# Kernel optimization log

Hardware: AMD Instinct MI355X
Metric: run time of the kernel (lower is better)

## Reference

```python
import jax, jax.numpy as jnp
import numpy as np

N = 8192
BOX = 50.0
CUTOFF = 5.0
MAX_E = 64 * N  # padded edge capacity (~34 avg neighbors expected)


def setup_inputs() -> dict:
    key = jax.random.key(0)
    pos = jax.random.uniform(key, (N, 3), dtype=jnp.float32) * BOX
    return {"pos": pos}


def _pairwise_dist(pos):
    # Euclidean cdist via the gram-matrix identity; avoids the [N,N,3] intermediate.
    sq = jnp.sum(pos * pos, axis=-1)                      # [N]
    d2 = sq[:, None] + sq[None, :] - 2.0 * (pos @ pos.T)  # [N,N]
    return jnp.sqrt(jnp.maximum(d2, 0.0))


def reference(pos):
    n = pos.shape[0]
    dist = _pairwise_dist(pos)
    # mask self-edges by pushing the diagonal above the cutoff (as in the torch code)
    dist = dist + (CUTOFF + 1.0) * jnp.eye(n, dtype=dist.dtype)
    mask = dist < CUTOFF
    # data-dependent nonzero -> fixed-size padded output for jit compatibility;
    # padded entries are filled with -1.
    rows, cols = jnp.nonzero(mask, size=MAX_E, fill_value=-1)
    return jnp.stack([rows, cols], axis=0)  # [2, MAX_E], int32
```

## Files before the change

### kernel.cpp

```cpp
#include <hip/hip_runtime.h>
#include <stdint.h>

#define N 8192
#define MAX_E (64 * N)
#define NCHUNK (N / 64)
#define NCOL1 9
#define NCELLS (NCOL1 * NCOL1 * NCOL1)
#define CAP 40
#define SCALE (9.0f / 50.0f)
#define POISON 0xAAAAAAAAu
#define M_WAVES 4
#define E_BLOCKS 256
#define E_ROWS 32

__device__ __forceinline__ float sq_exact(float x, float y, float z) {
    return __fadd_rn(__fadd_rn(__fmul_rn(x, x), __fmul_rn(y, y)), __fmul_rn(z, z));
}

__device__ __forceinline__ bool edge_pred(float xi, float yi, float zi, float sqi,
                                          const float4& pj) {
    float dot = __fmaf_rn(zi, pj.z, __fmaf_rn(yi, pj.y, __fmul_rn(xi, pj.x)));
    float d2  = __fmaf_rn(-2.0f, dot, __fadd_rn(sqi, pj.w));
    return d2 < 0x1.8ffffep+4f;
}

__device__ __forceinline__ int cell_of(float v) {
    int c = (int)(__fmul_rn(v, SCALE));
    return c > 8 ? 8 : c;
}

__device__ __forceinline__ int cell3_of(float x, float y, float z) {
    return (cell_of(x) * NCOL1 + cell_of(y)) * NCOL1 + cell_of(z);
}

__global__ __launch_bounds__(256) void bin_kernel(const float* __restrict__ posf,
                                                  unsigned* __restrict__ gcount,
                                                  float4* __restrict__ colpts,
                                                  int* __restrict__ colidx) {
    const int i = blockIdx.x * 256 + threadIdx.x;
    float x = posf[3 * i], y = posf[3 * i + 1], z = posf[3 * i + 2];
    const int cell = cell3_of(x, y, z);
    unsigned p = atomicAdd(&gcount[cell], 1u) - POISON;
    if (p < CAP) {
        colpts[cell * CAP + p] = make_float4(x, y, z, sq_exact(x, y, z));
        colidx[cell * CAP + p] = i;
    }
}

__global__ __launch_bounds__(256) void mask_kernel(const float* __restrict__ posf,
                                                   const unsigned* __restrict__ gcount,
                                                   const float4* __restrict__ colpts,
                                                   const int* __restrict__ colidx,
                                                   uint64_t* __restrict__ masks,
                                                   int* __restrict__ counts,
                                                   int* __restrict__ out) {
    __shared__ uint32_t lmask[M_WAVES][256];
    const int tid  = threadIdx.x;
    const int wave = tid >> 6;
    const int lane = tid & 63;
    const int row  = blockIdx.x * M_WAVES + wave;

    int2 neg; neg.x = -1; neg.y = -1;
    ((int2*)out)[blockIdx.x * 256 + tid] = neg;

#pragma unroll
    for (int k = lane; k < 256; k += 64) lmask[wave][k] = 0;
    __builtin_amdgcn_wave_barrier();

    const float xi = posf[3 * row], yi = posf[3 * row + 1], zi = posf[3 * row + 2];
    const float sqi = sq_exact(xi, yi, zi);
    const int cx = cell_of(xi), cy = cell_of(yi), cz = cell_of(zi);
    const int zlo = (cz > 0) ? cz - 1 : 0;
    const int zhi = (cz < 8) ? cz + 1 : 8;

    for (int dx = -1; dx <= 1; dx++) {
        const int nx = cx + dx;
        if ((unsigned)nx > 8u) continue;
        for (int dy = -1; dy <= 1; dy++) {
            const int ny = cy + dy;
            if ((unsigned)ny > 8u) continue;
            const int c0 = (nx * NCOL1 + ny) * NCOL1 + zlo;
            int l0 = (int)(gcount[c0] - POISON);     l0 = l0 > CAP ? CAP : l0;
            int l1 = (int)(gcount[c0 + 1] - POISON); l1 = l1 > CAP ? CAP : l1;
            int l2 = 0;
            if (zhi - zlo == 2) {
                l2 = (int)(gcount[c0 + 2] - POISON); l2 = l2 > CAP ? CAP : l2;
            }
            const int t01 = l0 + l1;
            const int tot = t01 + l2;
            for (int k = lane; k < tot; k += 64) {
                const int cellk = c0 + (k >= l0) + (k >= t01);
                const int off = k - ((k >= l0) ? l0 : 0) - ((k >= t01) ? l1 : 0);
                const int a = cellk * CAP + off;
                float4 pj = colpts[a];
                int j = colidx[a];
                if (j != row && edge_pred(xi, yi, zi, sqi, pj))
                    atomicOr(&lmask[wave][j >> 5], 1u << (j & 31));
            }
        }
    }
    __builtin_amdgcn_wave_barrier();

    uint4 u = ((const uint4*)lmask[wave])[lane];
    uint64_t k0 = (uint64_t)u.x | ((uint64_t)u.y << 32);
    uint64_t k1 = (uint64_t)u.z | ((uint64_t)u.w << 32);
    ulonglong2 v; v.x = k0; v.y = k1;
    ((ulonglong2*)(masks + (size_t)row * NCHUNK))[lane] = v;
    int t = __popcll(k0) + __popcll(k1);
#pragma unroll
    for (int o = 32; o > 0; o >>= 1) t += __shfl_down(t, o);
    if (lane == 0) counts[row] = t;
}

__global__ __launch_bounds__(256) void emit_kernel(const uint64_t* __restrict__ masks,
                                                   const int* __restrict__ counts,
                                                   int* __restrict__ out) {
    const int tid  = threadIdx.x;
    const int wave = tid >> 6;
    const int lane = tid & 63;
    const int row0 = blockIdx.x * E_ROWS;

    __shared__ int incl[256];
    __shared__ int wtot[4];
    __shared__ int excl32[32];

    const int4* c4 = (const int4*)counts;
    int s = 0;
#pragma unroll
    for (int k = 0; k < 8; k++) {
        int4 v = c4[tid * 8 + k];
        s += v.x + v.y + v.z + v.w;
    }
    int x = s;
#pragma unroll
    for (int o = 1; o < 64; o <<= 1) {
        int t = __shfl_up(x, o);
        if (lane >= o) x += t;
    }
    if (lane == 63) wtot[wave] = x;

    if (tid < 32) {
        int c = counts[row0 + tid];
        int y = c;
#pragma unroll
        for (int o = 1; o < 32; o <<= 1) {
            int t = __shfl_up(y, o, 32);
            if (tid >= o) y += t;
        }
        excl32[tid] = y - c;
    }
    __syncthreads();
    int woff = 0;
#pragma unroll
    for (int w = 0; w < 3; w++) woff += (wave > w) ? wtot[w] : 0;
    incl[tid] = woff + x;
    __syncthreads();
    const int base = (blockIdx.x > 0) ? incl[blockIdx.x - 1] : 0;

#pragma unroll
    for (int r = 0; r < 8; r++) {
        const int lr  = wave * 8 + r;
        const int row = row0 + lr;
        ulonglong2 v = ((const ulonglong2*)(masks + (size_t)row * NCHUNK))[lane];
        int s0 = __popcll(v.x), s1 = __popcll(v.y);
        int xs = s0 + s1;
#pragma unroll
        for (int o = 1; o < 64; o <<= 1) {
            int t = __shfl_up(xs, o);
            if (lane >= o) xs += t;
        }
        int slot = base + excl32[lr] + (xs - (s0 + s1));

        const int col0 = lane * 128;
        uint64_t m = v.x;
        while (m) {
            int b = __ffsll((unsigned long long)m) - 1;
            m &= m - 1;
            if (slot < MAX_E) { out[slot] = row; out[MAX_E + slot] = col0 + b; }
            slot++;
        }
        m = v.y;
        while (m) {
            int b = __ffsll((unsigned long long)m) - 1;
            m &= m - 1;
            if (slot < MAX_E) { out[slot] = row; out[MAX_E + slot] = col0 + 64 + b; }
            slot++;
        }
    }
}

extern "C" void kernel_launch(void* const* d_in, const int* in_sizes, int n_in,
                              void* d_out, int out_size, void* d_ws, size_t ws_size,
                              hipStream_t stream) {
    const float* posf = (const float*)d_in[0];
    int* out = (int*)d_out;
    char* ws = (char*)d_ws;
    int*      counts = (int*)ws;
    unsigned* gcount = (unsigned*)(ws + (64 << 10));
    int*      colidx = (int*)(ws + (128 << 10));
    float4*   colpts = (float4*)(ws + (256 << 10));
    uint64_t* masks  = (uint64_t*)(ws + (1 << 20));

    bin_kernel<<<N / 256, 256, 0, stream>>>(posf, gcount, colpts, colidx);
    mask_kernel<<<N / M_WAVES, 256, 0, stream>>>(posf, gcount, colpts, colidx,
                                                 masks, counts, out);
    emit_kernel<<<E_BLOCKS, 256, 0, stream>>>(masks, counts, out);
}
```

Measured before the change: 79.03 us.

## Stage compacted uint16 column lists in mask kernel instead of full bitmasks

The mask kernel now compacts each row's neighbor bitmask into a list of 16-bit column indices (capped at RCAP=128 per row) and writes it to a staging buffer. The emit kernel then copies those lists straight into the output, with no re-reading of 1 KB masks per row and no second scan. Bin data packs the particle index into the float4 w component, which drops the separate colidx array, and the squared norm of each neighbor is recomputed on the fly. This cuts global traffic between kernels. The risk is the silent truncation of rows with more than 128 neighbors and the serial bit-extraction loop moving into the mask kernel.

```diff
diff --git a/kernel.cpp b/kernel.cpp
--- a/kernel.cpp
+++ b/kernel.cpp
@@ -3,10 +3,10 @@
 
 #define N 8192
 #define MAX_E (64 * N)
-#define NCHUNK (N / 64)
 #define NCOL1 9
 #define NCELLS (NCOL1 * NCOL1 * NCOL1)
 #define CAP 40
+#define RCAP 128
 #define SCALE (9.0f / 50.0f)
 #define POISON 0xAAAAAAAAu
 #define M_WAVES 4
@@ -18,9 +18,10 @@
 }
 
 __device__ __forceinline__ bool edge_pred(float xi, float yi, float zi, float sqi,
-                                          const float4& pj) {
-    float dot = __fmaf_rn(zi, pj.z, __fmaf_rn(yi, pj.y, __fmul_rn(xi, pj.x)));
-    float d2  = __fmaf_rn(-2.0f, dot, __fadd_rn(sqi, pj.w));
+                                          float px, float py, float pz) {
+    float sqj = sq_exact(px, py, pz);
+    float dot = __fmaf_rn(zi, pz, __fmaf_rn(yi, py, __fmul_rn(xi, px)));
+    float d2  = __fmaf_rn(-2.0f, dot, __fadd_rn(sqi, sqj));
     return d2 < 0x1.8ffffep+4f;
 }
 
@@ -35,23 +36,20 @@
 
 __global__ __launch_bounds__(256) void bin_kernel(const float* __restrict__ posf,
                                                   unsigned* __restrict__ gcount,
-                                                  float4* __restrict__ colpts,
-                                                  int* __restrict__ colidx) {
+                                                  float4* __restrict__ colpts) {
     const int i = blockIdx.x * 256 + threadIdx.x;
     float x = posf[3 * i], y = posf[3 * i + 1], z = posf[3 * i + 2];
     const int cell = cell3_of(x, y, z);
     unsigned p = atomicAdd(&gcount[cell], 1u) - POISON;
     if (p < CAP) {
-        colpts[cell * CAP + p] = make_float4(x, y, z, sq_exact(x, y, z));
-        colidx[cell * CAP + p] = i;
+        colpts[cell * CAP + p] = make_float4(x, y, z, __int_as_float(i));
     }
 }
 
 __global__ __launch_bounds__(256) void mask_kernel(const float* __restrict__ posf,
                                                    const unsigned* __restrict__ gcount,
                                                    const float4* __restrict__ colpts,
-                                                   const int* __restrict__ colidx,
-                                                   uint64_t* __restrict__ masks,
+                                                   uint16_t* __restrict__ stage,
                                                    int* __restrict__ counts,
                                                    int* __restrict__ out) {
     __shared__ uint32_t lmask[M_WAVES][256];
@@ -91,10 +89,9 @@
             for (int k = lane; k < tot; k += 64) {
                 const int cellk = c0 + (k >= l0) + (k >= t01);
                 const int off = k - ((k >= l0) ? l0 : 0) - ((k >= t01) ? l1 : 0);
-                const int a = cellk * CAP + off;
-                float4 pj = colpts[a];
-                int j = colidx[a];
-                if (j != row && edge_pred(xi, yi, zi, sqi, pj))
+                float4 pj = colpts[cellk * CAP + off];
+                const int j = __float_as_int(pj.w);
+                if (j != row && edge_pred(xi, yi, zi, sqi, pj.x, pj.y, pj.z))
                     atomicOr(&lmask[wave][j >> 5], 1u << (j & 31));
             }
         }
@@ -104,15 +101,35 @@
     uint4 u = ((const uint4*)lmask[wave])[lane];
     uint64_t k0 = (uint64_t)u.x | ((uint64_t)u.y << 32);
     uint64_t k1 = (uint64_t)u.z | ((uint64_t)u.w << 32);
-    ulonglong2 v; v.x = k0; v.y = k1;
-    ((ulonglong2*)(masks + (size_t)row * NCHUNK))[lane] = v;
-    int t = __popcll(k0) + __popcll(k1);
-#pragma unroll
-    for (int o = 32; o > 0; o >>= 1) t += __shfl_down(t, o);
-    if (lane == 0) counts[row] = t;
-}
-
-__global__ __launch_bounds__(256) void emit_kernel(const uint64_t* __restrict__ masks,
+    const int pc = __popcll(k0) + __popcll(k1);
+    int xs = pc;
+#pragma unroll
+    for (int o = 1; o < 64; o <<= 1) {
+        int t = __shfl_up(xs, o);
+        if (lane >= o) xs += t;
+    }
+    if (lane == 63) counts[row] = xs;
+    int off = xs - pc;
+
+    uint16_t* dst = stage + (size_t)row * RCAP;
+    const int col0 = lane * 128;
+    uint64_t m = k0;
+    while (m) {
+        int b = __ffsll((unsigned long long)m) - 1;
+        m &= m - 1;
+        if (off < RCAP) dst[off] = (uint16_t)(col0 + b);
+        off++;
+    }
+    m = k1;
+    while (m) {
+        int b = __ffsll((unsigned long long)m) - 1;
+        m &= m - 1;
+        if (off < RCAP) dst[off] = (uint16_t)(col0 + 64 + b);
+        off++;
+    }
+}
+
+__global__ __launch_bounds__(256) void emit_kernel(const uint16_t* __restrict__ stage,
                                                    const int* __restrict__ counts,
                                                    int* __restrict__ out) {
     const int tid  = threadIdx.x;
@@ -161,30 +178,16 @@
     for (int r = 0; r < 8; r++) {
         const int lr  = wave * 8 + r;
         const int row = row0 + lr;
-        ulonglong2 v = ((const ulonglong2*)(masks + (size_t)row * NCHUNK))[lane];
-        int s0 = __popcll(v.x), s1 = __popcll(v.y);
-        int xs = s0 + s1;
-#pragma unroll
-        for (int o = 1; o < 64; o <<= 1) {
-            int t = __shfl_up(xs, o);
-            if (lane >= o) xs += t;
-        }
-        int slot = base + excl32[lr] + (xs - (s0 + s1));
-
-        const int col0 = lane * 128;
-        uint64_t m = v.x;
-        while (m) {
-            int b = __ffsll((unsigned long long)m) - 1;
-            m &= m - 1;
-            if (slot < MAX_E) { out[slot] = row; out[MAX_E + slot] = col0 + b; }
-            slot++;
-        }
-        m = v.y;
-        while (m) {
-            int b = __ffsll((unsigned long long)m) - 1;
-            m &= m - 1;
-            if (slot < MAX_E) { out[slot] = row; out[MAX_E + slot] = col0 + 64 + b; }
-            slot++;
+        int c = counts[row];
+        c = c > RCAP ? RCAP : c;
+        const int slot = base + excl32[lr];
+        const uint16_t* src = stage + (size_t)row * RCAP;
+        for (int k = lane; k < c; k += 64) {
+            const int sk = slot + k;
+            if (sk < MAX_E) {
+                out[sk] = row;
+                out[MAX_E + sk] = (int)src[k];
+            }
         }
     }
 }
@@ -197,12 +200,11 @@
     char* ws = (char*)d_ws;
     int*      counts = (int*)ws;
     unsigned* gcount = (unsigned*)(ws + (64 << 10));
-    int*      colidx = (int*)(ws + (128 << 10));
     float4*   colpts = (float4*)(ws + (256 << 10));
-    uint64_t* masks  = (uint64_t*)(ws + (1 << 20));
-
-    bin_kernel<<<N / 256, 256, 0, stream>>>(posf, gcount, colpts, colidx);
-    mask_kernel<<<N / M_WAVES, 256, 0, stream>>>(posf, gcount, colpts, colidx,
-                                                 masks, counts, out);
-    emit_kernel<<<E_BLOCKS, 256, 0, stream>>>(masks, counts, out);
-}
+    uint16_t* stage  = (uint16_t*)(ws + (1 << 20));
+
+    bin_kernel<<<N / 256, 256, 0, stream>>>(posf, gcount, colpts);
+    mask_kernel<<<N / M_WAVES, 256, 0, stream>>>(posf, gcount, colpts,
+                                                 stage, counts, out);
+    emit_kernel<<<E_BLOCKS, 256, 0, stream>>>(stage, counts, out);
+}
```

Result: faster. 74.52 us, median of 2 (-5.7%).
